# Kernel tuning notes

Measured on AMD Instinct MI355X. Metric: run time of the kernel, lower is better.

## Reference

```python
import jax, jax.numpy as jnp
import numpy as np

C = 256          # channels
D = C // 4       # q/k dim and angle-embedding hidden_dim
SIGMA = 15.0
BN_EPS = 1e-5
N_LAYERS = 4


def angle_embed(angles, proj_w, proj_b):
    """AngleEmbedding: sinusoidal PE (detached in torch) + Linear proj.
    angles [...,], returns [..., D]. Interleaved sin/cos matches the torch
    cat([sin,cos],dim=2).view(...) layout."""
    factor = 180.0 / (np.pi * SIGMA)
    idx = angles * factor
    div_term = jnp.exp(jnp.arange(0, D, 2, dtype=jnp.float32) * (-np.log(10000.0) / D))  # [D/2]
    om = idx[..., None] * div_term                                  # [..., D/2]
    emb = jnp.stack([jnp.sin(om), jnp.cos(om)], axis=-1).reshape(*angles.shape, D)
    emb = jax.lax.stop_gradient(emb)  # torch: embeddings.detach()
    return emb @ proj_w.T + proj_b


def sa_layer(x, pca, a_self, a_cross, Wq, Wk, Wv, Wvp, Wl, bl, bn_g, bn_b,
             p1w, p1b, p2w, p2b, beta_x, beta_w, picked):
    # x, pca: [B, C, N]
    xq = jnp.einsum('oc,bcn->bno', Wq, x)              # [B,N,D]  q_conv (tied to k_conv_pca)
    k_lrf = jnp.einsum('oc,bcn->bon', Wk, x)           # [B,D,N]
    k_pca = jnp.einsum('oc,bcn->bon', Wq, pca)         # [B,D,N]  weight-tied to q
    energy_lrf = jnp.einsum('bno,bom->bnm', xq, k_lrf)
    energy_pca = jnp.einsum('bno,bom->bnm', xq, k_pca)
    # relative-angle bias terms
    emb1 = angle_embed(a_self, p1w, p1b)               # [B,N,N,D]
    energy_lrf = energy_lrf + jnp.einsum('bnc,bnmc->bnm', xq, emb1)
    emb2 = angle_embed(a_cross, p2w, p2b)              # [B,N,D]
    energy_pca = energy_pca + jnp.einsum('bnc,bmc->bnm', xq, emb2)
    # learn_weight=True combination, softmax over last dim, then column renorm
    energy = jax.nn.softmax(beta_w * energy_lrf + (1.0 - beta_w) * energy_pca, axis=-1)
    energy = energy / (1e-12 + energy.sum(axis=1, keepdims=True))
    point_relation = energy[:, picked, :][:, None, :]  # [B,1,N]
    x_lrf = jnp.einsum('oc,bcn,bnm->bom', Wv, x, energy)
    x_pca = jnp.einsum('oc,bcn,bnm->bom', Wvp, pca, energy)
    x_r = beta_x * x_lrf + (1.0 - beta_x) * x_pca
    h = jnp.einsum('oc,bcn->bon', Wl, x - x_r) + bl[:, None]
    # BatchNorm1d in eval mode: running_mean=0, running_var=1
    h = h / jnp.sqrt(1.0 + BN_EPS) * bn_g[:, None] + bn_b[:, None]
    return x + jax.nn.gelu(h, approximate=False), point_relation


def forward(lrf, pca, angle_self, angle_cross, Wq, Wk, Wv, Wvp, Wl, bl,
            bn_g, bn_b, p1w, p1b, p2w, p2b, beta_x, beta_w, picked):
    x = lrf
    outs = []
    for i in range(N_LAYERS):
        x, _ = sa_layer(x, pca, angle_self, angle_cross, Wq[i], Wk[i], Wv[i],
                        Wvp[i], Wl[i], bl[i], bn_g[i], bn_b[i], p1w[i], p1b[i],
                        p2w[i], p2b[i], beta_x[i], beta_w[i], picked)
        outs.append(x)
    return jnp.concatenate(outs, axis=1)   # [B, 4*C, N]


def setup_inputs() -> dict:
    key = jax.random.key(0)
    ks = jax.random.split(key, 18)
    B, N, L = 64, 128, N_LAYERS
    s = 0.05
    return {
        'lrf': jax.random.normal(ks[0], (B, C, N), dtype=jnp.float32),
        'pca': jax.random.normal(ks[1], (B, C, N), dtype=jnp.float32),
        'angle_self': jax.random.uniform(ks[2], (B, N, N), dtype=jnp.float32),
        'angle_cross': jax.random.uniform(ks[3], (B, N), dtype=jnp.float32),
        'Wq': jax.random.normal(ks[4], (L, D, C)) * s,
        'Wk': jax.random.normal(ks[5], (L, D, C)) * s,
        'Wv': jax.random.normal(ks[6], (L, C, C)) * s,
        'Wvp': jax.random.normal(ks[7], (L, C, C)) * s,
        'Wl': jax.random.normal(ks[8], (L, C, C)) * s,
        'bl': jax.random.normal(ks[9], (L, C)) * s,
        'bn_g': jnp.ones((L, C), dtype=jnp.float32),
        'bn_b': jnp.zeros((L, C), dtype=jnp.float32),
        'p1w': jax.random.normal(ks[10], (L, D, D)) * s,
        'p1b': jax.random.normal(ks[11], (L, D)) * s,
        'p2w': jax.random.normal(ks[12], (L, D, D)) * s,
        'p2b': jax.random.normal(ks[13], (L, D)) * s,
        'beta_x': jnp.full((L,), 0.6, dtype=jnp.float32),
        'beta_w': jnp.full((L,), 0.6, dtype=jnp.float32),
        'picked': 0,
    }


def reference(lrf, pca, angle_self, angle_cross, Wq, Wk, Wv, Wvp, Wl, bl,
              bn_g, bn_b, p1w, p1b, p2w, p2b, beta_x, beta_w, picked):
    return forward(lrf, pca, angle_self, angle_cross, Wq, Wk, Wv, Wvp, Wl, bl,
                   bn_g, bn_b, p1w, p1b, p2w, p2b, beta_x, beta_w, picked)
```

## Files before the change

kernel.cpp:

```cpp
#include <hip/hip_runtime.h>
#include <cstdint>
#include <cstddef>


#define BB 64
#define CH 256
#define NP 128
#define DQ 64
#define NLAYERS 4

#define ANG_FACTOR 3.8197186342054885f
#define ANG_REV    0.6079271018540267f
#define DIV_STEP   0.28782313662425575f

#define LROW 264

typedef unsigned short u16;
typedef __attribute__((ext_vector_type(8))) short sh8;
typedef __attribute__((ext_vector_type(4))) float f32x4;
#define MFMA(a, b, c) __builtin_amdgcn_mfma_f32_16x16x32_bf16(a, b, c, 0, 0, 0)

static __device__ __forceinline__ u16 f2bf(float x) {
  unsigned u = __float_as_uint(x);
  return (u16)((u + 0x7FFFu + ((u >> 16) & 1u)) >> 16);
}
static __device__ __forceinline__ float bf2f(u16 h) {
  return __uint_as_float(((unsigned)h) << 16);
}
static __device__ __forceinline__ float hw_sin(float rev) {
  float r;
  asm("v_sin_f32 %0, %1" : "=v"(r) : "v"(rev));
  return r;
}
static __device__ __forceinline__ float hw_cos(float rev) {
  float r;
  asm("v_cos_f32 %0, %1" : "=v"(r) : "v"(rev));
  return r;
}

__global__ __launch_bounds__(256) void k_init(
    const float* __restrict__ Wv, const float* __restrict__ Wvp,
    const float* __restrict__ Wl, const float* __restrict__ Wq,
    const float* __restrict__ Wk, const float* __restrict__ p1w,
    const float* __restrict__ p2w, const float* __restrict__ pca,
    const float* __restrict__ lrf, const float* __restrict__ ac,
    u16* __restrict__ Wlbf, u16* __restrict__ Wqhi, u16* __restrict__ Wqlo,
    u16* __restrict__ Wkhi, u16* __restrict__ Wklo, u16* __restrict__ p1wT,
    u16* __restrict__ p2wbf, u16* __restrict__ pThi, u16* __restrict__ pTlo,
    u16* __restrict__ xThi, u16* __restrict__ xTlo,
    u16* __restrict__ WvT, u16* __restrict__ WvpT, u16* __restrict__ emb2bf)
{
  __shared__ __align__(16) float tl[64 * 65];
  int blk = blockIdx.x, tid = threadIdx.x;
  if (blk < 256) {
    int i = (blk * 256 + tid) * 4;
    float4 v = *(const float4*)(Wl + i);
    u16 o[4] = {f2bf(v.x), f2bf(v.y), f2bf(v.z), f2bf(v.w)};
    *(uint2*)(Wlbf + i) = *(const uint2*)o;
  } else if (blk < 384) {
    int bb = blk - 256;
    const float* s = (bb < 64) ? Wq : Wk;
    u16* dh = (bb < 64) ? Wqhi : Wkhi;
    u16* dl = (bb < 64) ? Wqlo : Wklo;
    int i = ((bb & 63) * 256 + tid) * 4;
    float4 v = *(const float4*)(s + i);
    float vv[4] = {v.x, v.y, v.z, v.w};
    u16 h[4], l[4];
#pragma unroll
    for (int r = 0; r < 4; r++) {
      h[r] = f2bf(vv[r]);
      l[r] = f2bf(vv[r] - bf2f(h[r]));
    }
    *(uint2*)(dh + i) = *(const uint2*)h;
    *(uint2*)(dl + i) = *(const uint2*)l;
  } else if (blk < 388) {
    int l = blk - 384;
    const float* src = p1w + (size_t)l * DQ * DQ;
    u16* dst = p1wT + (size_t)l * DQ * DQ;
#pragma unroll
    for (int i = 0; i < 16; i++) {
      int idx = tid + i * 256;
      int dd = idx >> 6, oo = idx & 63;
      dst[idx] = f2bf(src[oo * DQ + dd]);
    }
  } else if (blk < 392) {
    int l = blk - 388;
    const float* src = p2w + (size_t)l * DQ * DQ;
    u16* dst = p2wbf + (size_t)l * DQ * DQ;
#pragma unroll
    for (int i = 0; i < 16; i++) {
      int idx = tid + i * 256;
      dst[idx] = f2bf(src[idx]);
    }
  } else if (blk < 1416) {
    int bi = blk - 392;
    int nt = bi & 1, y = (bi >> 1) & 7, b = bi >> 4;
    int ct = y & 3, is_lrf = y >> 2;
    const float* x = is_lrf ? lrf : pca;
// ... 170 lines not shown
      }
    }
    {
      const u16* A20 = p2wbf + (size_t)l * DQ * DQ + ((size_t)(dt * 32) + lm) * DQ + lk * 8;
      const u16* A21 = A20 + 16 * DQ;
      const u16* B20 = emb2bf + ((size_t)b * NP + nt * 32 + lm) * DQ + lk * 8;
      const u16* B21 = B20 + 16 * DQ;
#pragma unroll
      for (int ks = 0; ks < 2; ks++) {
        int o = ks * 32;
        sh8 a0 = *(const sh8*)(A20 + o), a1 = *(const sh8*)(A21 + o);
        sh8 b0 = *(const sh8*)(B20 + o), b1 = *(const sh8*)(B21 + o);
        acc[0][0] = MFMA(a0, b0, acc[0][0]);
        acc[0][1] = MFMA(a0, b1, acc[0][1]);
        acc[1][0] = MFMA(a1, b0, acc[1][0]);
        acc[1][1] = MFMA(a1, b1, acc[1][1]);
      }
    }
#pragma unroll
    for (int i = 0; i < 2; i++)
#pragma unroll
      for (int j = 0; j < 2; j++) {
        int n = nt * 32 + j * 16 + lm;
        int d0 = dt * 32 + i * 16 + lk * 4;
        size_t off = (((size_t)l * BB + b) * NP + n) * DQ + d0;
        f32x4 v = acc[i][j];
        u16 h[4], lo[4];
#pragma unroll
        for (int r2 = 0; r2 < 4; r2++) {
          float vv = v[r2] + p2b[l * DQ + d0 + r2];
          h[r2] = f2bf(vv);
          lo[r2] = f2bf(vv - bf2f(h[r2]));
        }
        *(uint2*)&KP2hiA[off] = *(const uint2*)h;
        *(uint2*)&KP2loA[off] = *(const uint2*)lo;
      }
  } else {
    int bi = blockIdx.x - 512;
    int l = bi >> 9, rest = bi & 511;
    int ct = rest >> 6, b = rest & 63;
    int nt = tid >> 6;
    {
      const u16* sH = M2b + (size_t)l * CH * CH + (size_t)ct * 32 * CH;
      STAGE_W(WS, sH)
    }
    __syncthreads();
    const u16* X0 = pThi + ((size_t)b * NP + nt * 32 + lm) * CH + lk * 8;
    const u16* X1 = X0 + 16 * CH;
    f32x4 a00 = {}, a01 = {}, a10 = {}, a11 = {};
#pragma unroll
    for (int kb = 0; kb < 2; kb++) {
      sh8 rx0[4], rx1[4];
#pragma unroll
      for (int u = 0; u < 4; u++) {
        int o = (kb * 4 + u) * 32;
        rx0[u] = *(const sh8*)(X0 + o); rx1[u] = *(const sh8*)(X1 + o);
      }
#pragma unroll
      for (int u = 0; u < 4; u++) {
        int o2 = (kb * 4 + u) * 32 + lk * 8;
        sh8 w0 = *(const sh8*)&WS[lm * LROW + o2];
        sh8 w1 = *(const sh8*)&WS[(16 + lm) * LROW + o2];
        a00 = MFMA(w0, rx0[u], a00);
        a01 = MFMA(w0, rx1[u], a01);
        a10 = MFMA(w1, rx0[u], a10);
        a11 = MFMA(w1, rx1[u], a11);
      }
    }
    f32x4 acc[2][2] = {{a00, a01}, {a10, a11}};
#pragma unroll
    for (int i = 0; i < 2; i++)
#pragma unroll
      for (int j = 0; j < 2; j++) {
        int c0 = ct * 32 + i * 16 + lk * 4;
        int n = nt * 32 + j * 16 + lm;
        u16 ov[4];
#pragma unroll
        for (int r2 = 0; r2 < 4; r2++) ov[r2] = f2bf(acc[i][j][r2]);
        *(uint2*)&WlUPA[(((size_t)l * BB + b) * NP + n) * CH + c0] = *(const uint2*)ov;
      }
  }
}

__global__ __launch_bounds__(256) void k_qk(
    const u16* __restrict__ xThi, const u16* __restrict__ xTlo,
    const u16* __restrict__ Wqhi, const u16* __restrict__ Wqlo,
    const u16* __restrict__ Wkhi, const u16* __restrict__ Wklo,
    u16* __restrict__ XQhi, u16* __restrict__ XQlo,
    u16* __restrict__ KLThi, u16* __restrict__ KLTlo)
{
  __shared__ __align__(16) u16 WS[2 * 32 * LROW];
  int tid = threadIdx.x, lane = tid & 63, wave = tid >> 6;
  int lm = lane & 15, lk = lane >> 4;
  int bi = blockIdx.x;
  int mat = bi >> 8, r = bi & 255;
  int dt = r >> 7, r2 = r & 127;
  int nh = r2 >> 6, b = r2 & 63;
  u16* WH = WS;
  u16* WL = WS + 32 * LROW;
  {
    const u16* sH = (mat ? Wkhi : Wqhi) + (size_t)dt * 32 * CH;
    const u16* sL = (mat ? Wklo : Wqlo) + (size_t)dt * 32 * CH;
    STAGE_W(WH, sH)
    STAGE_W(WL, sL)
  }
  __syncthreads();
  int n0 = nh * 64 + wave * 16;
  const u16* B0h = xThi + ((size_t)b * NP + n0 + lm) * CH + lk * 8;
  const u16* B0l = xTlo + ((size_t)b * NP + n0 + lm) * CH + lk * 8;
  f32x4 acc[2] = {};
#pragma unroll
  for (int kb = 0; kb < 4; kb++) {
    sh8 rbh[2], rbl[2];
#pragma unroll
    for (int u = 0; u < 2; u++) {
      int o = (kb * 2 + u) * 32;
      rbh[u] = *(const sh8*)(B0h + o);
      rbl[u] = *(const sh8*)(B0l + o);
    }
#pragma unroll
    for (int u = 0; u < 2; u++) {
      int o2 = (kb * 2 + u) * 32 + lk * 8;
      sh8 a0h = *(const sh8*)&WH[lm * LROW + o2];
      sh8 a1h = *(const sh8*)&WH[(16 + lm) * LROW + o2];
      sh8 a0l = *(const sh8*)&WL[lm * LROW + o2];
      sh8 a1l = *(const sh8*)&WL[(16 + lm) * LROW + o2];
      acc[0] = MFMA(a0h, rbh[u], acc[0]);
      acc[0] = MFMA(a0h, rbl[u], acc[0]);
      acc[0] = MFMA(a0l, rbh[u], acc[0]);
      acc[1] = MFMA(a1h, rbh[u], acc[1]);
      acc[1] = MFMA(a1h, rbl[u], acc[1]);
      acc[1] = MFMA(a1l, rbh[u], acc[1]);
    }
  }
  int n = n0 + lm;
#pragma unroll
  for (int i = 0; i < 2; i++) {
    int d0 = dt * 32 + i * 16 + lk * 4;
    size_t off = ((size_t)b * NP + n) * DQ + d0;
    u16 h[4], lo[4];
#pragma unroll
    for (int r3 = 0; r3 < 4; r3++) {
      h[r3] = f2bf(acc[i][r3]);
      lo[r3] = f2bf(acc[i][r3] - bf2f(h[r3]));
    }
    if (mat == 0) {
      *(uint2*)&XQhi[off] = *(const uint2*)h;
      *(uint2*)&XQlo[off] = *(const uint2*)lo;
    } else {
      *(uint2*)&KLThi[off] = *(const uint2*)h;
      *(uint2*)&KLTlo[off] = *(const uint2*)lo;
    }
  }
}

__global__ __launch_bounds__(256) void k_att(
    const u16* __restrict__ XQhi, const u16* __restrict__ XQlo,
    const u16* __restrict__ KLThi, const u16* __restrict__ KLTlo,
    const u16* __restrict__ KP2hi, const u16* __restrict__ KP2lo,
    const u16* __restrict__ p1wT, const float* __restrict__ p1b,
    const float* __restrict__ AS, const float* __restrict__ beta_w, int layer,
    u16* __restrict__ PT, float* __restrict__ SCLp)
{
  __shared__ __align__(16) char smem[25856];
  int tid = threadIdx.x;
  int lane = tid & 63;
  int lm = lane & 15, lk = lane >> 4;
  int g = blockIdx.x & 3, b = blockIdx.x >> 2;
  int wave = tid >> 6;
  float* q1sh = (float*)smem;
  float* c1sh = q1sh + 32 * 66;
  float* divs = c1sh + 32;
  float* Esh  = divs + 32;
  if (tid < 32) divs[tid] = __expf(-(float)tid * DIV_STEP);
  float bw = beta_w[layer], obw = 1.0f - bw;
  {
    int mt = wave;
    size_t arow = ((size_t)b * NP + mt * 32 + lm) * DQ + lk * 8;
    size_t brow = ((size_t)b * NP + g * 32 + lm) * DQ + lk * 8;
    const u16* L0h = KLThi + arow;
    const u16* L0l = KLTlo + arow;
    const u16* P0h = KP2hi + arow;
    const u16* P0l = KP2lo + arow;
    const u16* X0h = XQhi + brow;
    const u16* X0l = XQlo + brow;
    sh8 xh[2][2], xl[2][2], lh[2][2], llr[2][2], ph[2][2], pl[2][2];
#pragma unroll
    for (int row = 0; row < 2; row++) {
#pragma unroll
      for (int ks = 0; ks < 2; ks++) {
        int o = row * 16 * DQ + ks * 32;
        xh[row][ks] = *(const sh8*)(X0h + o);
        xl[row][ks] = *(const sh8*)(X0l + o);
        lh[row][ks] = *(const sh8*)(L0h + o);
        llr[row][ks] = *(const sh8*)(L0l + o);
        ph[row][ks] = *(const sh8*)(P0h + o);
        pl[row][ks] = *(const sh8*)(P0l + o);
      }
    }
    f32x4 aL[2][2] = {};
    f32x4 aP[2][2] = {};
#pragma unroll
    for (int ks = 0; ks < 2; ks++) {
#pragma unroll
      for (int i = 0; i < 2; i++) {
#pragma unroll
        for (int j = 0; j < 2; j++) {
          aL[i][j] = MFMA(lh[i][ks], xh[j][ks], aL[i][j]);
          aL[i][j] = MFMA(lh[i][ks], xl[j][ks], aL[i][j]);
          aL[i][j] = MFMA(llr[i][ks], xh[j][ks], aL[i][j]);
          aP[i][j] = MFMA(ph[i][ks], xh[j][ks], aP[i][j]);
          aP[i][j] = MFMA(ph[i][ks], xl[j][ks], aP[i][j]);
          aP[i][j] = MFMA(pl[i][ks], xh[j][ks], aP[i][j]);
        }
      }
    }
#pragma unroll
    for (int i = 0; i < 2; i++)
#pragma unroll
      for (int j = 0; j < 2; j++) {
        int nloc = j * 16 + lm;
        int mloc = mt * 32 + i * 16 + lk * 4;
        float4 v;
        v.x = bw * aL[i][j][0] + obw * aP[i][j][0];
        v.y = bw * aL[i][j][1] + obw * aP[i][j][1];
        v.z = bw * aL[i][j][2] + obw * aP[i][j][2];
        v.w = bw * aL[i][j][3] + obw * aP[i][j][3];
        *(float4*)&Esh[nloc * 132 + mloc] = v;
      }
  }
  if (wave < 2) {
    const u16* A0 = XQhi + ((size_t)b * NP + g * 32 + lm) * DQ + lk * 8;
    const u16* A1 = A0 + 16 * DQ;
    const u16* B0 = p1wT + ((size_t)(wave * 32) + lm) * DQ + lk * 8;
    const u16* B1 = B0 + 16 * DQ;
    f32x4 q[2][2] = {};
#pragma unroll
    for (int ks = 0; ks < 2; ks++) {
      int o = ks * 32;
      sh8 a0 = *(const sh8*)(A0 + o), a1 = *(const sh8*)(A1 + o);
      sh8 b0 = *(const sh8*)(B0 + o), b1 = *(const sh8*)(B1 + o);
      q[0][0] = MFMA(a0, b0, q[0][0]);
      q[0][1] = MFMA(a0, b1, q[0][1]);
      q[1][0] = MFMA(a1, b0, q[1][0]);
      q[1][1] = MFMA(a1, b1, q[1][1]);
    }
#pragma unroll
    for (int i = 0; i < 2; i++)
#pragma unroll
      for (int j = 0; j < 2; j++)
#pragma unroll
        for (int r = 0; r < 4; r++)
          q1sh[(i * 16 + lk * 4 + r) * 66 + wave * 32 + j * 16 + lm] = q[i][j][r];
  }
  {
    int n = tid >> 3, o0 = (tid & 7) * 8;
    const u16* xs = XQhi + ((size_t)b * NP + g * 32 + n) * DQ + o0;
    uint2 w0 = *(const uint2*)xs;
    uint2 w1 = *(const uint2*)(xs + 4);
    const u16* hh = (const u16*)&w0;
    const u16* h2 = (const u16*)&w1;
    float s = 0.0f;
#pragma unroll
    for (int k = 0; k < 4; k++) s = fmaf(bf2f(hh[k]), p1b[o0 + k], s);
#pragma unroll
    for (int k = 0; k < 4; k++) s = fmaf(bf2f(h2[k]), p1b[o0 + 4 + k], s);
    s += __shfl_xor(s, 1);
    s += __shfl_xor(s, 2);
    s += __shfl_xor(s, 4);
    if ((tid & 7) == 0) c1sh[n] = s;
  }
  __syncthreads();
  {
    int n = tid >> 3, mc = (tid & 7) * 16;
    size_t asrow = ((size_t)b * NP + g * 32 + n) * NP + mc;
    float idxv[16], bias[16];
    float c1v = c1sh[n];
#pragma unroll
    for (int k4 = 0; k4 < 4; k4++) {
      float4 a4 = *(const float4*)&AS[asrow + k4 * 4];
      idxv[k4 * 4 + 0] = a4.x * ANG_REV;
      idxv[k4 * 4 + 1] = a4.y * ANG_REV;
      idxv[k4 * 4 + 2] = a4.z * ANG_REV;
      idxv[k4 * 4 + 3] = a4.w * ANG_REV;
    }
#pragma unroll
    for (int k = 0; k < 16; k++) bias[k] = c1v;
    for (int j = 0; j < 32; j++) {
      float dv = divs[j];
      float qs = q1sh[n * 66 + 2 * j], qc = q1sh[n * 66 + 2 * j + 1];
#pragma unroll
      for (int k = 0; k < 16; k++) {
        float rev = idxv[k] * dv;
        bias[k] = fmaf(qs, hw_sin(rev), bias[k]);
        bias[k] = fmaf(qc, hw_cos(rev), bias[k]);
      }
    }
    float ev[16], mx = -1e30f;
#pragma unroll
    for (int k = 0; k < 16; k++) {
      ev[k] = Esh[n * 132 + mc + k] + bw * bias[k];
      mx = fmaxf(mx, ev[k]);
    }
    mx = fmaxf(mx, __shfl_xor(mx, 1));
    mx = fmaxf(mx, __shfl_xor(mx, 2));
    mx = fmaxf(mx, __shfl_xor(mx, 4));
    float s = 0.0f;
#pragma unroll
    for (int k = 0; k < 16; k++) {
      ev[k] = __expf(ev[k] - mx);
      s += ev[k];
    }
    s += __shfl_xor(s, 1);
    s += __shfl_xor(s, 2);
    s += __shfl_xor(s, 4);
    float inv = 1.0f / s;
#pragma unroll
    for (int k = 0; k < 16; k++) Esh[n * 132 + mc + k] = ev[k] * inv;
  }
  __syncthreads();
  {
    int m = tid >> 1, nc = (tid & 1) * 16;
    float s = 0.0f;
    u16 tmp[16];
#pragma unroll
    for (int k = 0; k < 16; k++) {
      float v = Esh[(nc + k) * 132 + m];
      s += v;
      tmp[k] = f2bf(v);
    }
    u16* dst = PT + ((size_t)b * NP + m) * NP + g * 32 + nc;
    *(uint4*)&dst[0] = *(const uint4*)&tmp[0];
    *(uint4*)&dst[8] = *(const uint4*)&tmp[8];
    s += __shfl_xor(s, 1);
    if ((tid & 1) == 0) SCLp[((size_t)b * 4 + g) * NP + m] = s;
  }
}

__global__ __launch_bounds__(256) void k_h4(
    const u16* __restrict__ xThi, const u16* __restrict__ Mb,
    const u16* __restrict__ Wlbf, const u16* __restrict__ WlUP,
    const u16* __restrict__ PT, const float* __restrict__ SCLp,
    const float* __restrict__ bl, const float* __restrict__ bng,
    const float* __restrict__ bnb, const float* __restrict__ xsrc, int xbs,
    float* __restrict__ out, int layer,
    u16* __restrict__ xThi_o, u16* __restrict__ xTlo_o)
{
  __shared__ __align__(16) u16 WS[2 * 32 * LROW];
  int ct = blockIdx.x >> 6, b = blockIdx.x & 63;
  int tid = threadIdx.x, lane = tid & 63, wave = tid >> 6;
  int lm = lane & 15, lk = lane >> 4;
  u16* MT = WS;
  u16* WT = WS + 32 * LROW;
  {
    const u16* sM = Mb + (size_t)ct * 32 * CH;
    const u16* sW = Wlbf + (size_t)ct * 32 * CH;
    STAGE_W(MT, sM)
    STAGE_W(WT, sW)
  }
  __syncthreads();
  const u16* X0 = xThi + ((size_t)b * NP + wave * 32 + lm) * CH + lk * 8;
  const u16* X1 = X0 + 16 * CH;
  f32x4 awl[2][2] = {};
  f32x4 afp[2][2] = {};
#pragma unroll
  for (int kb = 0; kb < 2; kb++) {
    sh8 rx0[4], rx1[4];
#pragma unroll
    for (int u = 0; u < 4; u++) {
      int o = (kb * 4 + u) * 32;
      rx0[u] = *(const sh8*)(X0 + o);
      rx1[u] = *(const sh8*)(X1 + o);
    }
#pragma unroll
    for (int u = 0; u < 4; u++) {
      int o2 = (kb * 4 + u) * 32 + lk * 8;
      sh8 m0 = *(const sh8*)&MT[lm * LROW + o2];
      sh8 m1 = *(const sh8*)&MT[(16 + lm) * LROW + o2];
      sh8 w0 = *(const sh8*)&WT[lm * LROW + o2];
      sh8 w1 = *(const sh8*)&WT[(16 + lm) * LROW + o2];
      awl[0][0] = MFMA(m0, rx0[u], awl[0][0]);
      awl[0][1] = MFMA(m0, rx1[u], awl[0][1]);
      awl[1][0] = MFMA(m1, rx0[u], awl[1][0]);
      awl[1][1] = MFMA(m1, rx1[u], awl[1][1]);
      afp[0][0] = MFMA(w0, rx0[u], afp[0][0]);
      afp[0][1] = MFMA(w0, rx1[u], afp[0][1]);
      afp[1][0] = MFMA(w1, rx0[u], afp[1][0]);
      afp[1][1] = MFMA(w1, rx1[u], afp[1][1]);
    }
  }
  __syncthreads();
  u16* wluS = WS;
#pragma unroll
  for (int i = 0; i < 2; i++)
#pragma unroll
    for (int j = 0; j < 2; j++) {
      int cl = i * 16 + lk * 4;
      int n = wave * 32 + j * 16 + lm;
      uint2 up = *(const uint2*)&WlUP[((size_t)b * NP + n) * CH + ct * 32 + cl];
      const u16* uph = (const u16*)&up;
#pragma unroll
      for (int r = 0; r < 4; r++)
        wluS[(cl + r) * 136 + n] = f2bf(awl[i][j][r] + bf2f(uph[r]));
    }
  __syncthreads();
  const u16* B0 = PT + ((size_t)b * NP + wave * 32 + lm) * NP + lk * 8;
  const u16* B1 = B0 + 16 * NP;
  f32x4 acc2[2][2] = {};
#pragma unroll
  for (int ks = 0; ks < 4; ks++) {
    int o = ks * 32;
    sh8 b0 = *(const sh8*)(B0 + o);
    sh8 b1 = *(const sh8*)(B1 + o);
    int o2 = ks * 32 + lk * 8;
    sh8 a0 = *(const sh8*)&wluS[lm * 136 + o2];
    sh8 a1 = *(const sh8*)&wluS[(16 + lm) * 136 + o2];
    acc2[0][0] = MFMA(a0, b0, acc2[0][0]);
    acc2[0][1] = MFMA(a0, b1, acc2[0][1]);
    acc2[1][0] = MFMA(a1, b0, acc2[1][0]);
    acc2[1][1] = MFMA(a1, b1, acc2[1][1]);
  }
  const float rbn = 0.999995000037499687f;
#pragma unroll
  for (int i = 0; i < 2; i++)
#pragma unroll
    for (int j = 0; j < 2; j++) {
      int m = wave * 32 + j * 16 + lm;
      int cq = ct * 32 + i * 16 + lk * 4;
      const float* sp = SCLp + (size_t)b * 4 * NP + m;
      float scl = 1.0f / (1e-12f + sp[0] + sp[NP] + sp[2 * NP] + sp[3 * NP]);
      u16 hh[4], llv[4];
#pragma unroll
      for (int r = 0; r < 4; r++) {
        int c = cq + r;
        float h = afp[i][j][r] - acc2[i][j][r] * scl + bl[c];
        h = h * rbn * bng[c] + bnb[c];
        float gg = 0.5f * h * (1.0f + erff(h * 0.70710678118654752440f));
        float ov = xsrc[(size_t)b * xbs + (size_t)c * NP + m] + gg;
        out[((size_t)b * 4 * CH + (size_t)layer * CH + c) * NP + m] = ov;
        hh[r] = f2bf(ov);
        llv[r] = f2bf(ov - bf2f(hh[r]));
      }
      size_t xoff = ((size_t)b * NP + m) * CH + cq;
      *(uint2*)&xThi_o[xoff] = *(const uint2*)hh;
      *(uint2*)&xTlo_o[xoff] = *(const uint2*)llv;
    }
}

extern "C" void kernel_launch(void* const* d_in, const int* in_sizes, int n_in,
                              void* d_out, int out_size, void* d_ws, size_t ws_size,
                              hipStream_t stream)
{
  (void)in_sizes; (void)n_in; (void)out_size; (void)ws_size;
  const float* lrf     = (const float*)d_in[0];
  const float* pca     = (const float*)d_in[1];
  const float* a_self  = (const float*)d_in[2];
  const float* a_cross = (const float*)d_in[3];
  const float* Wq  = (const float*)d_in[4];
  const float* Wk  = (const float*)d_in[5];
  const float* Wv  = (const float*)d_in[6];
  const float* Wvp = (const float*)d_in[7];
  const float* Wl  = (const float*)d_in[8];
  const float* bl  = (const float*)d_in[9];
  const float* bng = (const float*)d_in[10];
  const float* bnb = (const float*)d_in[11];
  const float* p1w = (const float*)d_in[12];
  const float* p1b = (const float*)d_in[13];
  const float* p2w = (const float*)d_in[14];
  const float* p2b = (const float*)d_in[15];
  const float* beta_x = (const float*)d_in[16];
  const float* beta_w = (const float*)d_in[17];
  float* out = (float*)d_out;
  float* ws  = (float*)d_ws;

  const size_t QKN = (size_t)BB * NP * DQ;
  const size_t ENN = (size_t)BB * NP * NP;
  const size_t XCN = (size_t)BB * NP * CH;

  float* SCLp = ws;
  u16* up = (u16*)(SCLp + (size_t)BB * 4 * NP);
  u16* xThiA = up;  up += XCN;
  u16* xTloA = up;  up += XCN;
  u16* xThiB = up;  up += XCN;
  u16* xTloB = up;  up += XCN;
  u16* pThi = up;   up += XCN;
  u16* pTlo = up;   up += XCN;
  u16* XQhi = up;   up += QKN;
  u16* XQlo = up;   up += QKN;
  u16* KLThi = up;  up += QKN;
  u16* KLTlo = up;  up += QKN;
  u16* KP2hiA = up; up += (size_t)NLAYERS * QKN;
  u16* KP2loA = up; up += (size_t)NLAYERS * QKN;
  u16* WlUPA = up;  up += (size_t)NLAYERS * XCN;
  u16* PTbf = up;   up += ENN;
  u16* Wlbf = up;   up += (size_t)NLAYERS * CH * CH;
  u16* WvT = up;    up += (size_t)NLAYERS * CH * CH;
  u16* WvpT = up;   up += (size_t)NLAYERS * CH * CH;
  u16* Mb = up;     up += (size_t)NLAYERS * CH * CH;
  u16* M2b = up;    up += (size_t)NLAYERS * CH * CH;
  u16* Wqhi = up;   up += (size_t)NLAYERS * DQ * CH;
  u16* Wqlo = up;   up += (size_t)NLAYERS * DQ * CH;
  u16* Wkhi = up;   up += (size_t)NLAYERS * DQ * CH;
  u16* Wklo = up;   up += (size_t)NLAYERS * DQ * CH;
  u16* p1wT = up;   up += (size_t)NLAYERS * DQ * DQ;
  u16* p2wbf = up;  up += (size_t)NLAYERS * DQ * DQ;
  u16* emb2bf = up; up += QKN;

  k_init<<<dim3(2568), 256, 0, stream>>>(
      Wv, Wvp, Wl, Wq, Wk, p1w, p2w, pca, lrf, a_cross,
      Wlbf, Wqhi, Wqlo, Wkhi, Wklo, p1wT, p2wbf,
      pThi, pTlo, xThiA, xTloA, WvT, WvpT, emb2bf);
  k_mm<<<dim3(128), 256, 0, stream>>>(WvT, WvpT, Wlbf, beta_x, Mb, M2b);
  k_pre2<<<dim3(2560), 256, 0, stream>>>(
      pThi, pTlo, Wqhi, Wqlo, M2b, p2wbf, emb2bf, p2b,
      KP2hiA, KP2loA, WlUPA);

  for (int l = 0; l < NLAYERS; l++) {
    const float* xsrc = (l == 0) ? lrf : (out + (size_t)(l - 1) * CH * NP);
    int xbs = (l == 0) ? CH * NP : 4 * CH * NP;
    u16* xhi_in  = (l & 1) ? xThiB : xThiA;
    u16* xlo_in  = (l & 1) ? xTloB : xTloA;
    u16* xhi_out = (l & 1) ? xThiA : xThiB;
    u16* xlo_out = (l & 1) ? xTloA : xTloB;
    k_qk<<<dim3(512), 256, 0, stream>>>(
        xhi_in, xlo_in,
        Wqhi + (size_t)l * DQ * CH, Wqlo + (size_t)l * DQ * CH,
        Wkhi + (size_t)l * DQ * CH, Wklo + (size_t)l * DQ * CH,
        XQhi, XQlo, KLThi, KLTlo);
    k_att<<<dim3(256), 256, 0, stream>>>(
        XQhi, XQlo, KLThi, KLTlo,
        KP2hiA + (size_t)l * QKN, KP2loA + (size_t)l * QKN,
        p1wT + (size_t)l * DQ * DQ, p1b + (size_t)l * DQ,
        a_self, beta_w, l, PTbf, SCLp);
    k_h4<<<dim3(512), 256, 0, stream>>>(
        xhi_in, Mb + (size_t)l * CH * CH, Wlbf + (size_t)l * CH * CH,
        WlUPA + (size_t)l * XCN, PTbf, SCLp,
        bl + (size_t)l * CH, bng + (size_t)l * CH, bnb + (size_t)l * CH,
        xsrc, xbs, out, l, xhi_out, xlo_out);
  }
}
```

Measured before the change: 204.5 us.

## Move x-only GEMMs into qk kernel and split attention into 16-row blocks

The Mb·x and Wl·x products, which depend only on the layer input, move out of the final per-layer kernel into the q/k projection kernel as extra blocks. Their results go to workspace buffers (bf16 WlU, fp32 Afp). The attention kernel now processes 16 query rows per block instead of 32, doubling its grid to 512 blocks and halving shared memory. The aim is better occupancy and overlap across the serial per-layer kernels. The cost is extra global round-trips for WlU and Afp, including uncoalesced strided scalar stores, plus more partial column sums to reduce.

```diff
diff --git a/kernel.cpp b/kernel.cpp
--- a/kernel.cpp
+++ b/kernel.cpp
@@ -9,11 +9,11 @@
 #define DQ 64
 #define NLAYERS 4
 
-#define ANG_FACTOR 3.8197186342054885f
 #define ANG_REV    0.6079271018540267f
 #define DIV_STEP   0.28782313662425575f
 
 #define LROW 264
+#define LROW2 136
 
 typedef unsigned short u16;
 typedef __attribute__((ext_vector_type(8))) short sh8;
@@ -350,75 +350,136 @@
   }
 }
 
-__global__ __launch_bounds__(256) void k_qk(
+__global__ __launch_bounds__(256) void k_qkh(
     const u16* __restrict__ xThi, const u16* __restrict__ xTlo,
     const u16* __restrict__ Wqhi, const u16* __restrict__ Wqlo,
     const u16* __restrict__ Wkhi, const u16* __restrict__ Wklo,
+    const u16* __restrict__ Mb, const u16* __restrict__ Wlbf,
+    const u16* __restrict__ WlUP,
     u16* __restrict__ XQhi, u16* __restrict__ XQlo,
-    u16* __restrict__ KLThi, u16* __restrict__ KLTlo)
+    u16* __restrict__ KLThi, u16* __restrict__ KLTlo,
+    u16* __restrict__ WlU, float* __restrict__ Afp)
 {
   __shared__ __align__(16) u16 WS[2 * 32 * LROW];
   int tid = threadIdx.x, lane = tid & 63, wave = tid >> 6;
   int lm = lane & 15, lk = lane >> 4;
-  int bi = blockIdx.x;
-  int mat = bi >> 8, r = bi & 255;
-  int dt = r >> 7, r2 = r & 127;
-  int nh = r2 >> 6, b = r2 & 63;
-  u16* WH = WS;
-  u16* WL = WS + 32 * LROW;
-  {
-    const u16* sH = (mat ? Wkhi : Wqhi) + (size_t)dt * 32 * CH;
-    const u16* sL = (mat ? Wklo : Wqlo) + (size_t)dt * 32 * CH;
-    STAGE_W(WH, sH)
-    STAGE_W(WL, sL)
-  }
-  __syncthreads();
-  int n0 = nh * 64 + wave * 16;
-  const u16* B0h = xThi + ((size_t)b * NP + n0 + lm) * CH + lk * 8;
-  const u16* B0l = xTlo + ((size_t)b * NP + n0 + lm) * CH + lk * 8;
-  f32x4 acc[2] = {};
-#pragma unroll
-  for (int kb = 0; kb < 4; kb++) {
-    sh8 rbh[2], rbl[2];
-#pragma unroll
-    for (int u = 0; u < 2; u++) {
-      int o = (kb * 2 + u) * 32;
-      rbh[u] = *(const sh8*)(B0h + o);
-      rbl[u] = *(const sh8*)(B0l + o);
-    }
-#pragma unroll
-    for (int u = 0; u < 2; u++) {
-      int o2 = (kb * 2 + u) * 32 + lk * 8;
-      sh8 a0h = *(const sh8*)&WH[lm * LROW + o2];
-      sh8 a1h = *(const sh8*)&WH[(16 + lm) * LROW + o2];
-      sh8 a0l = *(const sh8*)&WL[lm * LROW + o2];
-      sh8 a1l = *(const sh8*)&WL[(16 + lm) * LROW + o2];
-      acc[0] = MFMA(a0h, rbh[u], acc[0]);
-      acc[0] = MFMA(a0h, rbl[u], acc[0]);
-      acc[0] = MFMA(a0l, rbh[u], acc[0]);
-      acc[1] = MFMA(a1h, rbh[u], acc[1]);
-      acc[1] = MFMA(a1h, rbl[u], acc[1]);
-      acc[1] = MFMA(a1l, rbh[u], acc[1]);
-    }
-  }
-  int n = n0 + lm;
-#pragma unroll
-  for (int i = 0; i < 2; i++) {
-    int d0 = dt * 32 + i * 16 + lk * 4;
-    size_t off = ((size_t)b * NP + n) * DQ + d0;
-    u16 h[4], lo[4];
-#pragma unroll
-    for (int r3 = 0; r3 < 4; r3++) {
-      h[r3] = f2bf(acc[i][r3]);
-      lo[r3] = f2bf(acc[i][r3] - bf2f(h[r3]));
-    }
-    if (mat == 0) {
-      *(uint2*)&XQhi[off] = *(const uint2*)h;
-      *(uint2*)&XQlo[off] = *(const uint2*)lo;
-    } else {
-      *(uint2*)&KLThi[off] = *(const uint2*)h;
-      *(uint2*)&KLTlo[off] = *(const uint2*)lo;
-    }
+  if (blockIdx.x < 512) {
+    int bi = blockIdx.x;
+    int mat = bi >> 8, r = bi & 255;
+    int dt = r >> 7, r2 = r & 127;
+    int nh = r2 >> 6, b = r2 & 63;
+    u16* WH = WS;
+    u16* WL = WS + 32 * LROW;
+    {
+      const u16* sH = (mat ? Wkhi : Wqhi) + (size_t)dt * 32 * CH;
+      const u16* sL = (mat ? Wklo : Wqlo) + (size_t)dt * 32 * CH;
+      STAGE_W(WH, sH)
+      STAGE_W(WL, sL)
+    }
+    __syncthreads();
+    int n0 = nh * 64 + wave * 16;
+    const u16* B0h = xThi + ((size_t)b * NP + n0 + lm) * CH + lk * 8;
+    const u16* B0l = xTlo + ((size_t)b * NP + n0 + lm) * CH + lk * 8;
+    f32x4 acc[2] = {};
+#pragma unroll
+    for (int kb = 0; kb < 4; kb++) {
+      sh8 rbh[2], rbl[2];
+#pragma unroll
+      for (int u = 0; u < 2; u++) {
+        int o = (kb * 2 + u) * 32;
+        rbh[u] = *(const sh8*)(B0h + o);
+        rbl[u] = *(const sh8*)(B0l + o);
+      }
+#pragma unroll
+      for (int u = 0; u < 2; u++) {
+        int o2 = (kb * 2 + u) * 32 + lk * 8;
+        sh8 a0h = *(const sh8*)&WH[lm * LROW + o2];
+        sh8 a1h = *(const sh8*)&WH[(16 + lm) * LROW + o2];
+        sh8 a0l = *(const sh8*)&WL[lm * LROW + o2];
+        sh8 a1l = *(const sh8*)&WL[(16 + lm) * LROW + o2];
+        acc[0] = MFMA(a0h, rbh[u], acc[0]);
+        acc[0] = MFMA(a0h, rbl[u], acc[0]);
+        acc[0] = MFMA(a0l, rbh[u], acc[0]);
+        acc[1] = MFMA(a1h, rbh[u], acc[1]);
+        acc[1] = MFMA(a1h, rbl[u], acc[1]);
+        acc[1] = MFMA(a1l, rbh[u], acc[1]);
+      }
+    }
+    int n = n0 + lm;
+#pragma unroll
+    for (int i = 0; i < 2; i++) {
+      int d0 = dt * 32 + i * 16 + lk * 4;
+      size_t off = ((size_t)b * NP + n) * DQ + d0;
+      u16 h[4], lo[4];
+#pragma unroll
+      for (int r3 = 0; r3 < 4; r3++) {
+        h[r3] = f2bf(acc[i][r3]);
+        lo[r3] = f2bf(acc[i][r3] - bf2f(h[r3]));
+      }
+      if (mat == 0) {
+        *(uint2*)&XQhi[off] = *(const uint2*)h;
+        *(uint2*)&XQlo[off] = *(const uint2*)lo;
+      } else {
+        *(uint2*)&KLThi[off] = *(const uint2*)h;
+        *(uint2*)&KLTlo[off] = *(const uint2*)lo;
+      }
+    }
+  } else {
+    int bi = blockIdx.x - 512;
+    int ct = bi >> 6, b = bi & 63;
+    u16* MT = WS;
+    u16* WT = WS + 32 * LROW;
+    {
+      const u16* sM = Mb + (size_t)ct * 32 * CH;
+      const u16* sW = Wlbf + (size_t)ct * 32 * CH;
+      STAGE_W(MT, sM)
+      STAGE_W(WT, sW)
+    }
+    __syncthreads();
+    const u16* X0 = xThi + ((size_t)b * NP + wave * 32 + lm) * CH + lk * 8;
+    const u16* X1 = X0 + 16 * CH;
+    f32x4 awl[2][2] = {};
+    f32x4 afp[2][2] = {};
+#pragma unroll
+    for (int kb = 0; kb < 2; kb++) {
+      sh8 rx0[4], rx1[4];
+#pragma unroll
+      for (int u = 0; u < 4; u++) {
+        int o = (kb * 4 + u) * 32;
+        rx0[u] = *(const sh8*)(X0 + o);
+        rx1[u] = *(const sh8*)(X1 + o);
+      }
+#pragma unroll
+      for (int u = 0; u < 4; u++) {
+        int o2 = (kb * 4 + u) * 32 + lk * 8;
+        sh8 m0 = *(const sh8*)&MT[lm * LROW + o2];
+        sh8 m1 = *(const sh8*)&MT[(16 + lm) * LROW + o2];
+        sh8 w0 = *(const sh8*)&WT[lm * LROW + o2];
+        sh8 w1 = *(const sh8*)&WT[(16 + lm) * LROW + o2];
+        awl[0][0] = MFMA(m0, rx0[u], awl[0][0]);
+        awl[0][1] = MFMA(m0, rx1[u], awl[0][1]);
+        awl[1][0] = MFMA(m1, rx0[u], awl[1][0]);
+        awl[1][1] = MFMA(m1, rx1[u], awl[1][1]);
+        afp[0][0] = MFMA(w0, rx0[u], afp[0][0]);
+        afp[0][1] = MFMA(w0, rx1[u], afp[0][1]);
+        afp[1][0] = MFMA(w1, rx0[u], afp[1][0]);
+        afp[1][1] = MFMA(w1, rx1[u], afp[1][1]);
+      }
+    }
+#pragma unroll
+    for (int i = 0; i < 2; i++)
+#pragma unroll
+      for (int j = 0; j < 2; j++) {
+        int cl = ct * 32 + i * 16 + lk * 4;
+        int n = wave * 32 + j * 16 + lm;
+        uint2 up = *(const uint2*)&WlUP[((size_t)b * NP + n) * CH + cl];
+        const u16* uph = (const u16*)&up;
+#pragma unroll
+        for (int r = 0; r < 4; r++) {
+          WlU[((size_t)b * CH + cl + r) * NP + n] = f2bf(awl[i][j][r] + bf2f(uph[r]));
+          Afp[((size_t)b * CH + cl + r) * NP + n] = afp[i][j][r];
+        }
+      }
   }
 }
 
@@ -430,122 +491,108 @@
     const float* __restrict__ AS, const float* __restrict__ beta_w, int layer,
     u16* __restrict__ PT, float* __restrict__ SCLp)
 {
-  __shared__ __align__(16) char smem[25856];
+  __shared__ __align__(16) char smem[13056];
   int tid = threadIdx.x;
   int lane = tid & 63;
   int lm = lane & 15, lk = lane >> 4;
-  int g = blockIdx.x & 3, b = blockIdx.x >> 2;
+  int g8 = blockIdx.x & 7, b = blockIdx.x >> 3;
   int wave = tid >> 6;
+  int n0 = g8 * 16;
   float* q1sh = (float*)smem;
-  float* c1sh = q1sh + 32 * 66;
-  float* divs = c1sh + 32;
+  float* c1sh = q1sh + 16 * 66;
+  float* divs = c1sh + 16;
   float* Esh  = divs + 32;
   if (tid < 32) divs[tid] = __expf(-(float)tid * DIV_STEP);
   float bw = beta_w[layer], obw = 1.0f - bw;
   {
     int mt = wave;
     size_t arow = ((size_t)b * NP + mt * 32 + lm) * DQ + lk * 8;
-    size_t brow = ((size_t)b * NP + g * 32 + lm) * DQ + lk * 8;
+    size_t brow = ((size_t)b * NP + n0 + lm) * DQ + lk * 8;
     const u16* L0h = KLThi + arow;
     const u16* L0l = KLTlo + arow;
     const u16* P0h = KP2hi + arow;
     const u16* P0l = KP2lo + arow;
     const u16* X0h = XQhi + brow;
     const u16* X0l = XQlo + brow;
-    sh8 xh[2][2], xl[2][2], lh[2][2], llr[2][2], ph[2][2], pl[2][2];
-#pragma unroll
-    for (int row = 0; row < 2; row++) {
-#pragma unroll
-      for (int ks = 0; ks < 2; ks++) {
-        int o = row * 16 * DQ + ks * 32;
-        xh[row][ks] = *(const sh8*)(X0h + o);
-        xl[row][ks] = *(const sh8*)(X0l + o);
-        lh[row][ks] = *(const sh8*)(L0h + o);
-        llr[row][ks] = *(const sh8*)(L0l + o);
-        ph[row][ks] = *(const sh8*)(P0h + o);
-        pl[row][ks] = *(const sh8*)(P0l + o);
-      }
-    }
-    f32x4 aL[2][2] = {};
-    f32x4 aP[2][2] = {};
+    sh8 xh[2], xl[2], lh[2][2], llr[2][2], ph[2][2], pl[2][2];
 #pragma unroll
     for (int ks = 0; ks < 2; ks++) {
+      int o = ks * 32;
+      xh[ks] = *(const sh8*)(X0h + o);
+      xl[ks] = *(const sh8*)(X0l + o);
+#pragma unroll
+      for (int row = 0; row < 2; row++) {
+        int o2 = row * 16 * DQ + o;
+        lh[row][ks] = *(const sh8*)(L0h + o2);
+        llr[row][ks] = *(const sh8*)(L0l + o2);
+        ph[row][ks] = *(const sh8*)(P0h + o2);
+        pl[row][ks] = *(const sh8*)(P0l + o2);
+      }
+    }
+    f32x4 aL[2] = {};
+    f32x4 aP[2] = {};
+#pragma unroll
+    for (int ks = 0; ks < 2; ks++) {
 #pragma unroll
       for (int i = 0; i < 2; i++) {
-#pragma unroll
-        for (int j = 0; j < 2; j++) {
-          aL[i][j] = MFMA(lh[i][ks], xh[j][ks], aL[i][j]);
-          aL[i][j] = MFMA(lh[i][ks], xl[j][ks], aL[i][j]);
-          aL[i][j] = MFMA(llr[i][ks], xh[j][ks], aL[i][j]);
-          aP[i][j] = MFMA(ph[i][ks], xh[j][ks], aP[i][j]);
-          aP[i][j] = MFMA(ph[i][ks], xl[j][ks], aP[i][j]);
-          aP[i][j] = MFMA(pl[i][ks], xh[j][ks], aP[i][j]);
-        }
-      }
-    }
-#pragma unroll
-    for (int i = 0; i < 2; i++)
-#pragma unroll
-      for (int j = 0; j < 2; j++) {
-        int nloc = j * 16 + lm;
-        int mloc = mt * 32 + i * 16 + lk * 4;
-        float4 v;
-        v.x = bw * aL[i][j][0] + obw * aP[i][j][0];
-        v.y = bw * aL[i][j][1] + obw * aP[i][j][1];
-        v.z = bw * aL[i][j][2] + obw * aP[i][j][2];
-        v.w = bw * aL[i][j][3] + obw * aP[i][j][3];
-        *(float4*)&Esh[nloc * 132 + mloc] = v;
-      }
+        aL[i] = MFMA(lh[i][ks], xh[ks], aL[i]);
+        aL[i] = MFMA(lh[i][ks], xl[ks], aL[i]);
+        aL[i] = MFMA(llr[i][ks], xh[ks], aL[i]);
+        aP[i] = MFMA(ph[i][ks], xh[ks], aP[i]);
+        aP[i] = MFMA(ph[i][ks], xl[ks], aP[i]);
+        aP[i] = MFMA(pl[i][ks], xh[ks], aP[i]);
+      }
+    }
+#pragma unroll
+    for (int i = 0; i < 2; i++) {
+#pragma unroll
+      for (int r = 0; r < 4; r++) {
+        int mloc = mt * 32 + i * 16 + lk * 4 + r;
+        Esh[lm * 132 + mloc] = bw * aL[i][r] + obw * aP[i][r];
+      }
+    }
   }
   if (wave < 2) {
-    const u16* A0 = XQhi + ((size_t)b * NP + g * 32 + lm) * DQ + lk * 8;
-    const u16* A1 = A0 + 16 * DQ;
+    const u16* A0 = XQhi + ((size_t)b * NP + n0 + lm) * DQ + lk * 8;
     const u16* B0 = p1wT + ((size_t)(wave * 32) + lm) * DQ + lk * 8;
     const u16* B1 = B0 + 16 * DQ;
-    f32x4 q[2][2] = {};
+    f32x4 q[2] = {};
 #pragma unroll
     for (int ks = 0; ks < 2; ks++) {
       int o = ks * 32;
-      sh8 a0 = *(const sh8*)(A0 + o), a1 = *(const sh8*)(A1 + o);
+      sh8 a0 = *(const sh8*)(A0 + o);
       sh8 b0 = *(const sh8*)(B0 + o), b1 = *(const sh8*)(B1 + o);
-      q[0][0] = MFMA(a0, b0, q[0][0]);
-      q[0][1] = MFMA(a0, b1, q[0][1]);
-      q[1][0] = MFMA(a1, b0, q[1][0]);
-      q[1][1] = MFMA(a1, b1, q[1][1]);
-    }
-#pragma unroll
-    for (int i = 0; i < 2; i++)
-#pragma unroll
-      for (int j = 0; j < 2; j++)
-#pragma unroll
-        for (int r = 0; r < 4; r++)
-          q1sh[(i * 16 + lk * 4 + r) * 66 + wave * 32 + j * 16 + lm] = q[i][j][r];
+      q[0] = MFMA(a0, b0, q[0]);
+      q[1] = MFMA(a0, b1, q[1]);
+    }
+#pragma unroll
+    for (int j = 0; j < 2; j++)
+#pragma unroll
+      for (int r = 0; r < 4; r++)
+        q1sh[(lk * 4 + r) * 66 + wave * 32 + j * 16 + lm] = q[j][r];
   }
   {
-    int n = tid >> 3, o0 = (tid & 7) * 8;
-    const u16* xs = XQhi + ((size_t)b * NP + g * 32 + n) * DQ + o0;
+    int n = tid >> 4, o0 = (tid & 15) * 4;
+    const u16* xs = XQhi + ((size_t)b * NP + n0 + n) * DQ + o0;
     uint2 w0 = *(const uint2*)xs;
-    uint2 w1 = *(const uint2*)(xs + 4);
     const u16* hh = (const u16*)&w0;
-    const u16* h2 = (const u16*)&w1;
     float s = 0.0f;
 #pragma unroll
     for (int k = 0; k < 4; k++) s = fmaf(bf2f(hh[k]), p1b[o0 + k], s);
-#pragma unroll
-    for (int k = 0; k < 4; k++) s = fmaf(bf2f(h2[k]), p1b[o0 + 4 + k], s);
     s += __shfl_xor(s, 1);
     s += __shfl_xor(s, 2);
     s += __shfl_xor(s, 4);
-    if ((tid & 7) == 0) c1sh[n] = s;
+    s += __shfl_xor(s, 8);
+    if ((tid & 15) == 0) c1sh[n] = s;
   }
   __syncthreads();
   {
-    int n = tid >> 3, mc = (tid & 7) * 16;
-    size_t asrow = ((size_t)b * NP + g * 32 + n) * NP + mc;
-    float idxv[16], bias[16];
+    int n = tid >> 4, mc = (tid & 15) * 8;
+    size_t asrow = ((size_t)b * NP + n0 + n) * NP + mc;
+    float idxv[8], bias[8];
     float c1v = c1sh[n];
 #pragma unroll
-    for (int k4 = 0; k4 < 4; k4++) {
+    for (int k4 = 0; k4 < 2; k4++) {
       float4 a4 = *(const float4*)&AS[asrow + k4 * 4];
       idxv[k4 * 4 + 0] = a4.x * ANG_REV;
       idxv[k4 * 4 + 1] = a4.y * ANG_REV;
@@ -553,141 +600,101 @@
       idxv[k4 * 4 + 3] = a4.w * ANG_REV;
     }
 #pragma unroll
-    for (int k = 0; k < 16; k++) bias[k] = c1v;
+    for (int k = 0; k < 8; k++) bias[k] = c1v;
     for (int j = 0; j < 32; j++) {
       float dv = divs[j];
       float qs = q1sh[n * 66 + 2 * j], qc = q1sh[n * 66 + 2 * j + 1];
 #pragma unroll
-      for (int k = 0; k < 16; k++) {
+      for (int k = 0; k < 8; k++) {
         float rev = idxv[k] * dv;
         bias[k] = fmaf(qs, hw_sin(rev), bias[k]);
         bias[k] = fmaf(qc, hw_cos(rev), bias[k]);
       }
     }
-    float ev[16], mx = -1e30f;
-#pragma unroll
-    for (int k = 0; k < 16; k++) {
+    float ev[8], mx = -1e30f;
+#pragma unroll
+    for (int k = 0; k < 8; k++) {
       ev[k] = Esh[n * 132 + mc + k] + bw * bias[k];
       mx = fmaxf(mx, ev[k]);
     }
     mx = fmaxf(mx, __shfl_xor(mx, 1));
     mx = fmaxf(mx, __shfl_xor(mx, 2));
     mx = fmaxf(mx, __shfl_xor(mx, 4));
+    mx = fmaxf(mx, __shfl_xor(mx, 8));
     float s = 0.0f;
 #pragma unroll
-    for (int k = 0; k < 16; k++) {
+    for (int k = 0; k < 8; k++) {
       ev[k] = __expf(ev[k] - mx);
       s += ev[k];
     }
     s += __shfl_xor(s, 1);
     s += __shfl_xor(s, 2);
     s += __shfl_xor(s, 4);
+    s += __shfl_xor(s, 8);
     float inv = 1.0f / s;
 #pragma unroll
-    for (int k = 0; k < 16; k++) Esh[n * 132 + mc + k] = ev[k] * inv;
+    for (int k = 0; k < 8; k++) Esh[n * 132 + mc + k] = ev[k] * inv;
   }
   __syncthreads();
   {
-    int m = tid >> 1, nc = (tid & 1) * 16;
+    int m = tid >> 1, nc = (tid & 1) * 8;
     float s = 0.0f;
-    u16 tmp[16];
-#pragma unroll
-    for (int k = 0; k < 16; k++) {
+    u16 tmp[8];
+#pragma unroll
+    for (int k = 0; k < 8; k++) {
       float v = Esh[(nc + k) * 132 + m];
       s += v;
       tmp[k] = f2bf(v);
     }
-    u16* dst = PT + ((size_t)b * NP + m) * NP + g * 32 + nc;
+    u16* dst = PT + ((size_t)b * NP + m) * NP + n0 + nc;
     *(uint4*)&dst[0] = *(const uint4*)&tmp[0];
-    *(uint4*)&dst[8] = *(const uint4*)&tmp[8];
     s += __shfl_xor(s, 1);
-    if ((tid & 1) == 0) SCLp[((size_t)b * 4 + g) * NP + m] = s;
-  }
-}
-
-__global__ __launch_bounds__(256) void k_h4(
-    const u16* __restrict__ xThi, const u16* __restrict__ Mb,
-    const u16* __restrict__ Wlbf, const u16* __restrict__ WlUP,
-    const u16* __restrict__ PT, const float* __restrict__ SCLp,
+    if ((tid & 1) == 0) SCLp[((size_t)b * 8 + g8) * NP + m] = s;
+  }
+}
+
+__global__ __launch_bounds__(256) void k_h5(
+    const u16* __restrict__ WlU, const u16* __restrict__ PT,
+    const float* __restrict__ SCLp, const float* __restrict__ Afp,
     const float* __restrict__ bl, const float* __restrict__ bng,
     const float* __restrict__ bnb, const float* __restrict__ xsrc, int xbs,
     float* __restrict__ out, int layer,
     u16* __restrict__ xThi_o, u16* __restrict__ xTlo_o)
 {
-  __shared__ __align__(16) u16 WS[2 * 32 * LROW];
+  __shared__ __align__(16) u16 WS2[32 * LROW2];
   int ct = blockIdx.x >> 6, b = blockIdx.x & 63;
   int tid = threadIdx.x, lane = tid & 63, wave = tid >> 6;
   int lm = lane & 15, lk = lane >> 4;
-  u16* MT = WS;
-  u16* WT = WS + 32 * LROW;
   {
-    const u16* sM = Mb + (size_t)ct * 32 * CH;
-    const u16* sW = Wlbf + (size_t)ct * 32 * CH;
-    STAGE_W(MT, sM)
-    STAGE_W(WT, sW)
-  }
-  __syncthreads();
-  const u16* X0 = xThi + ((size_t)b * NP + wave * 32 + lm) * CH + lk * 8;
-  const u16* X1 = X0 + 16 * CH;
-  f32x4 awl[2][2] = {};
-  f32x4 afp[2][2] = {};
-#pragma unroll
-  for (int kb = 0; kb < 2; kb++) {
-    sh8 rx0[4], rx1[4];
-#pragma unroll
-    for (int u = 0; u < 4; u++) {
-      int o = (kb * 4 + u) * 32;
-      rx0[u] = *(const sh8*)(X0 + o);
-      rx1[u] = *(const sh8*)(X1 + o);
-    }
-#pragma unroll
-    for (int u = 0; u < 4; u++) {
-      int o2 = (kb * 4 + u) * 32 + lk * 8;
-      sh8 m0 = *(const sh8*)&MT[lm * LROW + o2];
-      sh8 m1 = *(const sh8*)&MT[(16 + lm) * LROW + o2];
-      sh8 w0 = *(const sh8*)&WT[lm * LROW + o2];
-      sh8 w1 = *(const sh8*)&WT[(16 + lm) * LROW + o2];
-      awl[0][0] = MFMA(m0, rx0[u], awl[0][0]);
-      awl[0][1] = MFMA(m0, rx1[u], awl[0][1]);
-      awl[1][0] = MFMA(m1, rx0[u], awl[1][0]);
-      awl[1][1] = MFMA(m1, rx1[u], awl[1][1]);
-      afp[0][0] = MFMA(w0, rx0[u], afp[0][0]);
-      afp[0][1] = MFMA(w0, rx1[u], afp[0][1]);
-      afp[1][0] = MFMA(w1, rx0[u], afp[1][0]);
-      afp[1][1] = MFMA(w1, rx1[u], afp[1][1]);
-    }
-  }
-  __syncthreads();
-  u16* wluS = WS;
-#pragma unroll
-  for (int i = 0; i < 2; i++)
-#pragma unroll
-    for (int j = 0; j < 2; j++) {
-      int cl = i * 16 + lk * 4;
-      int n = wave * 32 + j * 16 + lm;
-      uint2 up = *(const uint2*)&WlUP[((size_t)b * NP + n) * CH + ct * 32 + cl];
-      const u16* uph = (const u16*)&up;
-#pragma unroll
-      for (int r = 0; r < 4; r++)
-        wluS[(cl + r) * 136 + n] = f2bf(awl[i][j][r] + bf2f(uph[r]));
-    }
+    const u16* src = WlU + ((size_t)b * CH + ct * 32) * NP;
+#pragma unroll
+    for (int it = 0; it < 2; it++) {
+      int idx = tid + it * 256, row = idx >> 4, chq = idx & 15;
+      *(uint4*)&WS2[row * LROW2 + chq * 8] = *(const uint4*)(src + row * NP + chq * 8);
+    }
+  }
   __syncthreads();
   const u16* B0 = PT + ((size_t)b * NP + wave * 32 + lm) * NP + lk * 8;
   const u16* B1 = B0 + 16 * NP;
-  f32x4 acc2[2][2] = {};
+  sh8 rB0[4], rB1[4];
 #pragma unroll
   for (int ks = 0; ks < 4; ks++) {
     int o = ks * 32;
-    sh8 b0 = *(const sh8*)(B0 + o);
-    sh8 b1 = *(const sh8*)(B1 + o);
+    rB0[ks] = *(const sh8*)(B0 + o);
+    rB1[ks] = *(const sh8*)(B1 + o);
+  }
+  f32x4 a00 = {}, a01 = {}, a10 = {}, a11 = {};
+#pragma unroll
+  for (int ks = 0; ks < 4; ks++) {
     int o2 = ks * 32 + lk * 8;
-    sh8 a0 = *(const sh8*)&wluS[lm * 136 + o2];
-    sh8 a1 = *(const sh8*)&wluS[(16 + lm) * 136 + o2];
-    acc2[0][0] = MFMA(a0, b0, acc2[0][0]);
-    acc2[0][1] = MFMA(a0, b1, acc2[0][1]);
-    acc2[1][0] = MFMA(a1, b0, acc2[1][0]);
-    acc2[1][1] = MFMA(a1, b1, acc2[1][1]);
-  }
+    sh8 w0 = *(const sh8*)&WS2[lm * LROW2 + o2];
+    sh8 w1 = *(const sh8*)&WS2[(16 + lm) * LROW2 + o2];
+    a00 = MFMA(w0, rB0[ks], a00);
+    a01 = MFMA(w0, rB1[ks], a01);
+    a10 = MFMA(w1, rB0[ks], a10);
+    a11 = MFMA(w1, rB1[ks], a11);
+  }
+  f32x4 acc2[2][2] = {{a00, a01}, {a10, a11}};
   const float rbn = 0.999995000037499687f;
 #pragma unroll
   for (int i = 0; i < 2; i++)
@@ -695,13 +702,15 @@
     for (int j = 0; j < 2; j++) {
       int m = wave * 32 + j * 16 + lm;
       int cq = ct * 32 + i * 16 + lk * 4;
-      const float* sp = SCLp + (size_t)b * 4 * NP + m;
-      float scl = 1.0f / (1e-12f + sp[0] + sp[NP] + sp[2 * NP] + sp[3 * NP]);
+      const float* sp = SCLp + (size_t)b * 8 * NP + m;
+      float scl = 1.0f / (1e-12f + sp[0] + sp[NP] + sp[2 * NP] + sp[3 * NP] +
+                          sp[4 * NP] + sp[5 * NP] + sp[6 * NP] + sp[7 * NP]);
       u16 hh[4], llv[4];
 #pragma unroll
       for (int r = 0; r < 4; r++) {
         int c = cq + r;
-        float h = afp[i][j][r] - acc2[i][j][r] * scl + bl[c];
+        float a = Afp[((size_t)b * CH + c) * NP + m];
+        float h = a - acc2[i][j][r] * scl + bl[c];
         h = h * rbn * bng[c] + bnb[c];
         float gg = 0.5f * h * (1.0f + erff(h * 0.70710678118654752440f));
         float ov = xsrc[(size_t)b * xbs + (size_t)c * NP + m] + gg;
@@ -746,7 +755,8 @@
   const size_t XCN = (size_t)BB * NP * CH;
 
   float* SCLp = ws;
-  u16* up = (u16*)(SCLp + (size_t)BB * 4 * NP);
+  float* Afp  = SCLp + (size_t)BB * 8 * NP;
+  u16* up = (u16*)(Afp + (size_t)BB * CH * NP);
   u16* xThiA = up;  up += XCN;
   u16* xTloA = up;  up += XCN;
   u16* xThiB = up;  up += XCN;
@@ -760,6 +770,7 @@
   u16* KP2hiA = up; up += (size_t)NLAYERS * QKN;
   u16* KP2loA = up; up += (size_t)NLAYERS * QKN;
   u16* WlUPA = up;  up += (size_t)NLAYERS * XCN;
+  u16* WlUb = up;   up += XCN;
   u16* PTbf = up;   up += ENN;
   u16* Wlbf = up;   up += (size_t)NLAYERS * CH * CH;
   u16* WvT = up;    up += (size_t)NLAYERS * CH * CH;
@@ -790,20 +801,20 @@
     u16* xlo_in  = (l & 1) ? xTloB : xTloA;
     u16* xhi_out = (l & 1) ? xThiA : xThiB;
     u16* xlo_out = (l & 1) ? xTloA : xTloB;
-    k_qk<<<dim3(512), 256, 0, stream>>>(
+    k_qkh<<<dim3(1024), 256, 0, stream>>>(
         xhi_in, xlo_in,
         Wqhi + (size_t)l * DQ * CH, Wqlo + (size_t)l * DQ * CH,
         Wkhi + (size_t)l * DQ * CH, Wklo + (size_t)l * DQ * CH,
-        XQhi, XQlo, KLThi, KLTlo);
-    k_att<<<dim3(256), 256, 0, stream>>>(
+        Mb + (size_t)l * CH * CH, Wlbf + (size_t)l * CH * CH,
+        WlUPA + (size_t)l * XCN,
+        XQhi, XQlo, KLThi, KLTlo, WlUb, Afp);
+    k_att<<<dim3(512), 256, 0, stream>>>(
         XQhi, XQlo, KLThi, KLTlo,
         KP2hiA + (size_t)l * QKN, KP2loA + (size_t)l * QKN,
         p1wT + (size_t)l * DQ * DQ, p1b + (size_t)l * DQ,
         a_self, beta_w, l, PTbf, SCLp);
-    k_h4<<<dim3(512), 256, 0, stream>>>(
-        xhi_in, Mb + (size_t)l * CH * CH, Wlbf + (size_t)l * CH * CH,
-        WlUPA + (size_t)l * XCN, PTbf, SCLp,
-        bl + (size_t)l * CH, bng + (size_t)l * CH, bnb + (size_t)l * CH,
-        xsrc, xbs, out, l, xhi_out, xlo_out);
-  }
-}
+    k_h5<<<dim3(512), 256, 0, stream>>>(
+        WlUb, PTbf, SCLp, Afp, bl + (size_t)l * CH, bng + (size_t)l * CH,
+        bnb + (size_t)l * CH, xsrc, xbs, out, l, xhi_out, xlo_out);
+  }
+}
```

Result: slower. 218.5 us (+6.8%).
